# Optimization experiments

Measured on AMD Instinct MI355X. Metric: run time of the kernel, lower is better.

Reference implementation:

```python
import jax, jax.numpy as jnp
import numpy as np

B, N, D, H, C = 32, 128, 5000, 256, 4  # trees, nodes/tree, input_size_rumor, hidden, rumor_classes


def setup_inputs() -> dict:
    key = jax.random.key(0)
    ks = jax.random.split(key, 24)
    scale = 0.05  # xavier-like scale (module calls init_weight with xavier_uniform_)
    inp = {"x": jax.random.normal(ks[0], (B, N, D), dtype=jnp.float32)}
    names = ["Er", "Wsr_r", "Usr_r", "Wsr_z", "Usr_z", "Wsr_h", "Usr_h",
             "Wr_r", "Ur_r", "Usr2r_r", "Wr_z", "Ur_z", "Usr2r_z",
             "Wr_h", "Ur_h", "Usr2r_h"]
    shapes = [(H, D)] + [(H, H)] * 15
    for i, (n, s) in enumerate(zip(names, shapes)):
        inp[n] = jax.random.normal(ks[i + 1], s, dtype=jnp.float32) * scale
    inp["Vr"] = jax.random.normal(ks[17], (C, H), dtype=jnp.float32) * scale
    inp["br"] = jnp.zeros((C, 1), dtype=jnp.float32)
    # Tree structure: nodes in topological order; slot 0 = zero initial state,
    # node j is stored at slot j+1, parents[:, i] is the SLOT of node i's parent.
    rng = np.random.default_rng(0)
    pslot = np.zeros((B, N), dtype=np.int64)  # root's parent slot = 0 (zeros)
    for i in range(1, N):
        pslot[:, i] = rng.integers(1, i + 1, size=B)  # parent is an earlier node
    has_child = np.zeros((B, N), dtype=bool)
    for i in range(1, N):
        has_child[np.arange(B), pslot[:, i] - 1] = True
    inp["parents"] = jnp.asarray(pslot)
    inp["is_leaf"] = jnp.asarray(~has_child)
    return inp


def _tree_gru(x_tilde, parents, Wsr_r, Usr_r, Wsr_z, Usr_z, Wsr_h, Usr_h,
              Wr_r, Ur_r, Usr2r_r, Wr_z, Ur_z, Usr2r_z, Wr_h, Ur_h, Usr2r_h):
    """x_tilde: [B,N,H] embedded node features; parents: [B,N] parent SLOT ids.
    Returns h_rumor for every node: [B,N,H]. Same math as MultiModel.rumor_forward,
    with the Python recursion replaced by a scan over topologically-ordered nodes,
    vectorized across the batch of trees."""
    Bq, Nq, Hq = x_tilde.shape
    S0 = jnp.zeros((Bq, Nq + 1, Hq), x_tilde.dtype)  # slot 0 = initial zero state

    def step(carry, xs):
        S_sh, S_ru = carry  # [B, N+1, H] stored shared/rumor states
        xt, p, i = xs       # xt: [B,H], p: [B] parent slot, i: node index
        idx = p[:, None, None]
        hsp = jnp.take_along_axis(S_sh, idx, axis=1)[:, 0]  # [B,H] parent shared state
        hrp = jnp.take_along_axis(S_ru, idx, axis=1)[:, 0]  # [B,H] parent rumor state
        # shared GRU cell
        r_sh = jax.nn.sigmoid(xt @ Wsr_r.T + hsp @ Usr_r.T)
        z_sh = jax.nn.sigmoid(xt @ Wsr_z.T + hsp @ Usr_z.T)
        h_sh_t = jnp.tanh(xt @ Wsr_h.T + (hsp * r_sh) @ Usr_h.T)
        h_sh = (1 - z_sh) * hsp + z_sh * h_sh_t
        # rumor GRU cell (conditioned on shared state)
        r_ru = jax.nn.sigmoid(xt @ Wr_r.T + hrp @ Ur_r.T + h_sh @ Usr2r_r.T)
        z_ru = jax.nn.sigmoid(xt @ Wr_z.T + hrp @ Ur_z.T + h_sh @ Usr2r_z.T)
        h_ru_t = jnp.tanh(xt @ Wr_h.T + (hrp * r_ru) @ Ur_h.T + h_sh @ Usr2r_h.T)
        h_ru = (1 - z_ru) * hrp + z_ru * h_ru_t
        S_sh = S_sh.at[:, i + 1, :].set(h_sh)
        S_ru = S_ru.at[:, i + 1, :].set(h_ru)
        return (S_sh, S_ru), None

    xs = (jnp.swapaxes(x_tilde, 0, 1), parents.T, jnp.arange(Nq))
    (S_sh, S_ru), _ = jax.lax.scan(step, (S0, S0), xs)
    return S_ru[:, 1:, :]


def reference(x, Er, Wsr_r, Usr_r, Wsr_z, Usr_z, Wsr_h, Usr_h,
              Wr_r, Ur_r, Usr2r_r, Wr_z, Ur_z, Usr2r_z, Wr_h, Ur_h, Usr2r_h,
              Vr, br, parents, is_leaf):
    x_tilde = jnp.einsum('bnd,hd->bnh', x, Er)  # Er @ x for every node
    H_ru = _tree_gru(x_tilde, parents, Wsr_r, Usr_r, Wsr_z, Usr_z, Wsr_h, Usr_h,
                     Wr_r, Ur_r, Usr2r_r, Wr_z, Ur_z, Usr2r_z, Wr_h, Ur_h, Usr2r_h)
    # max over leaf node hidden vectors (torch.max over cat of leaf vectors)
    neg = jnp.finfo(H_ru.dtype).min
    hmax = jnp.where(is_leaf[:, :, None], H_ru, neg).max(axis=1)  # [B,H]
    logits = hmax @ Vr.T + br[:, 0]  # [B,C]
    return jax.nn.softmax(logits, axis=-1)
```

## Files before the change

### kernel.cpp

```cpp
#include <hip/hip_runtime.h>
#include <hip/hip_bf16.h>
#include <math.h>


#define H_DIM 256
#define N_NODES 128
#define B_TREES 32
#define MAXL 128
#define TPB 2
#define GRID_WGS 512

typedef short bf16x8 __attribute__((ext_vector_type(8)));
typedef float f32x4 __attribute__((ext_vector_type(4)));

__device__ __forceinline__ float sigmoidf_(float x) {
    return 1.0f / (1.0f + expf(-x));
}
__device__ __forceinline__ unsigned bfp(float x) {
    unsigned u = __float_as_uint(x);
    return (u + 0x7fffu + ((u >> 16) & 1u)) >> 16;
}
__device__ __forceinline__ float bflo(unsigned w) { return __uint_as_float(w << 16); }
__device__ __forceinline__ float bfhi(unsigned w) { return __uint_as_float(w & 0xffff0000u); }

__device__ __forceinline__ void unpack8(uint4 v, float* f) {
    f[0] = bflo(v.x); f[1] = bfhi(v.x);
    f[2] = bflo(v.y); f[3] = bfhi(v.y);
    f[4] = bflo(v.z); f[5] = bfhi(v.z);
    f[6] = bflo(v.w); f[7] = bfhi(v.w);
}

__device__ __forceinline__ float coh_load(const float* p) {
    return __hip_atomic_load(p, __ATOMIC_RELAXED, __HIP_MEMORY_SCOPE_AGENT);
}
__device__ __forceinline__ void coh_store(float* p, float v) {
    __hip_atomic_store(p, v, __ATOMIC_RELAXED, __HIP_MEMORY_SCOPE_AGENT);
}
__device__ __forceinline__ unsigned coh_loadu(const unsigned* p) {
    return __hip_atomic_load(p, __ATOMIC_RELAXED, __HIP_MEMORY_SCOPE_AGENT);
}
__device__ __forceinline__ void coh_storeu(unsigned* p, unsigned v) {
    __hip_atomic_store(p, v, __ATOMIC_RELAXED, __HIP_MEMORY_SCOPE_AGENT);
}

__global__ __launch_bounds__(256) void gemm_mfma_nt(
    const float* __restrict__ A, const float* __restrict__ B,
    float* __restrict__ C, int K, int ldc, int Kc, int zStride) {
    __shared__ short As[64][40];
    __shared__ short Bs[64][40];
    const int tid = threadIdx.x;
    const int bm = blockIdx.x, bn = blockIdx.y;
    const int z = blockIdx.z;
    const int k_begin = z * Kc;
    const int k_end = (k_begin + Kc < K) ? (k_begin + Kc) : K;
    float* Cz = C + (size_t)z * zStride;
    const int row = tid >> 2;
    const int quad = tid & 3;
    const int wave = tid >> 6;
    const int lane = tid & 63;
    const int lm = lane & 15;
    const int kq = lane >> 4;

    f32x4 acc[4];
#pragma unroll
    for (int i = 0; i < 4; ++i) acc[i] = (f32x4){0.f, 0.f, 0.f, 0.f};

    for (int k0 = k_begin; k0 < k_end; k0 += 32) {
        const int kbase = k0 + quad * 8;
        {
            float a8[8];
            const float* Ap = A + (size_t)(bm * 64 + row) * K + kbase;
            if (kbase + 8 <= k_end) {
                const float4 v0 = *(const float4*)Ap;
                const float4 v1 = *(const float4*)(Ap + 4);
                a8[0] = v0.x; a8[1] = v0.y; a8[2] = v0.z; a8[3] = v0.w;
                a8[4] = v1.x; a8[5] = v1.y; a8[6] = v1.z; a8[7] = v1.w;
            } else {
#pragma unroll
                for (int i = 0; i < 8; ++i)
                    a8[i] = (kbase + i < k_end) ? Ap[i] : 0.f;
            }
            uint4 v;
            v.x = bfp(a8[0]) | (bfp(a8[1]) << 16);
            v.y = bfp(a8[2]) | (bfp(a8[3]) << 16);
            v.z = bfp(a8[4]) | (bfp(a8[5]) << 16);
            v.w = bfp(a8[6]) | (bfp(a8[7]) << 16);
            *(uint4*)&As[row][quad * 8] = v;
        }
        {
            float b8[8];
            const float* Bp = B + (size_t)(bn * 64 + row) * K + kbase;
            if (kbase + 8 <= k_end) {
                const float4 v0 = *(const float4*)Bp;
                const float4 v1 = *(const float4*)(Bp + 4);
                b8[0] = v0.x; b8[1] = v0.y; b8[2] = v0.z; b8[3] = v0.w;
                b8[4] = v1.x; b8[5] = v1.y; b8[6] = v1.z; b8[7] = v1.w;
            } else {
#pragma unroll
                for (int i = 0; i < 8; ++i)
                    b8[i] = (kbase + i < k_end) ? Bp[i] : 0.f;
            }
            uint4 v;
            v.x = bfp(b8[0]) | (bfp(b8[1]) << 16);
            v.y = bfp(b8[2]) | (bfp(b8[3]) << 16);
            v.z = bfp(b8[4]) | (bfp(b8[5]) << 16);
            v.w = bfp(b8[6]) | (bfp(b8[7]) << 16);
            *(uint4*)&Bs[row][quad * 8] = v;
        }
        __syncthreads();
        const bf16x8 af = *(const bf16x8*)&As[wave * 16 + lm][kq * 8];
#pragma unroll
        for (int nt = 0; nt < 4; ++nt) {
            const bf16x8 bf = *(const bf16x8*)&Bs[nt * 16 + lm][kq * 8];
            acc[nt] = __builtin_amdgcn_mfma_f32_16x16x32_bf16(af, bf, acc[nt], 0, 0, 0);
        }
        __syncthreads();
    }
#pragma unroll
    for (int nt = 0; nt < 4; ++nt) {
#pragma unroll
        for (int r = 0; r < 4; ++r) {
            const int gm = bm * 64 + wave * 16 + kq * 4 + r;
            const int gn = bn * 64 + nt * 16 + lm;
            Cz[(size_t)gm * ldc + gn] = acc[nt][r];
        }
    }
}

__global__ __launch_bounds__(256) void gemm_mfma_w6(
    const float* __restrict__ A,
    const float* __restrict__ B0, const float* __restrict__ B1,
    const float* __restrict__ B2, const float* __restrict__ B3,
    const float* __restrict__ B4, const float* __restrict__ B5,
    float* __restrict__ C, int ldc) {
    __shared__ short As[64][40];
    __shared__ short Bs[64][40];
    const int tid = threadIdx.x;
    const int bm = blockIdx.x, bn = blockIdx.y;
    const float* Bsel[6] = {B0, B1, B2, B3, B4, B5};
    const int row = tid >> 2;
    const int quad = tid & 3;
    const int wave = tid >> 6;
    const int lane = tid & 63;
    const int lm = lane & 15;
    const int kq = lane >> 4;
    const float* Brow = Bsel[bn >> 2] + (size_t)((bn & 3) * 64 + row) * 256;
    const float* Arow = A + (size_t)(bm * 64 + row) * 256;

    f32x4 acc[4];
#pragma unroll
    for (int i = 0; i < 4; ++i) acc[i] = (f32x4){0.f, 0.f, 0.f, 0.f};

#pragma unroll
    for (int kt = 0; kt < 8; ++kt) {
        const int kbase = kt * 32 + quad * 8;
        {
            const float4 v0 = *(const float4*)(Arow + kbase);
            const float4 v1 = *(const float4*)(Arow + kbase + 4);
            uint4 v;
            v.x = bfp(v0.x) | (bfp(v0.y) << 16);
            v.y = bfp(v0.z) | (bfp(v0.w) << 16);
            v.z = bfp(v1.x) | (bfp(v1.y) << 16);
            v.w = bfp(v1.z) | (bfp(v1.w) << 16);
            *(uint4*)&As[row][quad * 8] = v;
        }
        {
            const float4 v0 = *(const float4*)(Brow + kbase);
            const float4 v1 = *(const float4*)(Brow + kbase + 4);
            uint4 v;
            v.x = bfp(v0.x) | (bfp(v0.y) << 16);
            v.y = bfp(v0.z) | (bfp(v0.w) << 16);
            v.z = bfp(v1.x) | (bfp(v1.y) << 16);
            v.w = bfp(v1.z) | (bfp(v1.w) << 16);
            *(uint4*)&Bs[row][quad * 8] = v;
        }
        __syncthreads();
        const bf16x8 af = *(const bf16x8*)&As[wave * 16 + lm][kq * 8];
#pragma unroll
        for (int nt = 0; nt < 4; ++nt) {
            const bf16x8 bf = *(const bf16x8*)&Bs[nt * 16 + lm][kq * 8];
            acc[nt] = __builtin_amdgcn_mfma_f32_16x16x32_bf16(af, bf, acc[nt], 0, 0, 0);
        }
        __syncthreads();
    }
#pragma unroll
    for (int nt = 0; nt < 4; ++nt) {
#pragma unroll
        for (int r = 0; r < 4; ++r) {
            const int gm = bm * 64 + wave * 16 + kq * 4 + r;
            const int gn = bn * 64 + nt * 16 + lm;
            C[(size_t)gm * ldc + gn] = acc[nt][r];
        }
    }
}

__global__ __launch_bounds__(256) void reduce4_k(
    const float* __restrict__ Pp, float* __restrict__ xt) {
    const int i = (blockIdx.x * 256 + threadIdx.x) * 4;
    const float4 a = *(const float4*)(Pp + i);
    const float4 b = *(const float4*)(Pp + 1048576 + i);
    const float4 c = *(const float4*)(Pp + 2097152 + i);
    const float4 d = *(const float4*)(Pp + 3145728 + i);
    float4 s;
    s.x = a.x + b.x + c.x + d.x;
    s.y = a.y + b.y + c.y + d.y;
    s.z = a.z + b.z + c.z + d.z;
    s.w = a.w + b.w + c.w + d.w;
    *(float4*)(xt + i) = s;
}

__global__ __launch_bounds__(256) void transpose_pack_u(
    const float* __restrict__ U0, const float* __restrict__ U1,
    const float* __restrict__ U2, const float* __restrict__ U3,
    const float* __restrict__ U4, const float* __restrict__ U5,
    const float* __restrict__ U6, const float* __restrict__ U7,
    const float* __restrict__ U8, uint4* __restrict__ UTb) {
    const float* Us[9] = {U0, U1, U2, U3, U4, U5, U6, U7, U8};
    const int jb = blockIdx.x;
    const int m = blockIdx.y;
    const int h = threadIdx.x;
    const float* U = Us[m] + (size_t)h * 256 + jb * 8;
    uint4 v;
    v.x = bfp(U[0]) | (bfp(U[1]) << 16);
    v.y = bfp(U[2]) | (bfp(U[3]) << 16);
    v.z = bfp(U[4]) | (bfp(U[5]) << 16);
    v.w = bfp(U[6]) | (bfp(U[7]) << 16);
    UTb[(size_t)(m * 32 + jb) * 256 + h] = v;
}

__global__ __launch_bounds__(256) void build_schedule(
    const int* __restrict__ parents, int* __restrict__ sched,
    int* __restrict__ level_off, int* __restrict__ gstart,
    int* __restrict__ gend, int* __restrict__ ngrp,
    unsigned* __restrict__ ready) {
    __shared__ unsigned char depth[B_TREES][N_NODES];
    __shared__ int counts[MAXL];
    __shared__ int base[MAXL + 1];
    const int tid = threadIdx.x;
    for (int k = tid; k < B_TREES * N_NODES; k += 256)
        coh_storeu(&ready[k], 0u);
    for (int k = tid; k < MAXL; k += 256) counts[k] = 0;
    __syncthreads();
    if (tid < B_TREES) {
        depth[tid][0] = 0;
        for (int i = 1; i < N_NODES; ++i) {
            const int p = parents[tid * N_NODES + i];
            depth[tid][i] = (unsigned char)(depth[tid][p - 1] + 1);
        }
    }
    __syncthreads();
    for (int k = tid; k < B_TREES * N_NODES; k += 256)
        atomicAdd(&counts[depth[k >> 7][k & 127]], 1);
    __syncthreads();
    if (tid == 0) {
        int acc = 0;
        int nl = 0;
        for (int l = 0; l < MAXL; ++l) {
            base[l] = acc;
            acc += counts[l];
            if (counts[l] > 0) nl = l + 1;
        }
        base[MAXL] = acc;
        level_off[MAXL + 1] = nl;
        int ng = 0;
        for (int l = 0; l < nl; ++l) {
            for (int s = base[l]; s < base[l + 1]; s += TPB) {
                gstart[ng] = s;
                gend[ng] = (s + TPB < base[l + 1]) ? s + TPB : base[l + 1];
                ++ng;
            }
        }
        *ngrp = ng;
    }
    __syncthreads();
    for (int k = tid; k <= MAXL; k += 256) level_off[k] = base[k];
    for (int k = tid; k < MAXL; k += 256) counts[k] = 0;
    __syncthreads();
    for (int k = tid; k < B_TREES * N_NODES; k += 256) {
        const int d = depth[k >> 7][k & 127];
        const int pos = base[d] + atomicAdd(&counts[d], 1);
        sched[pos] = k;
    }
}

__global__ __launch_bounds__(256, 2) void tree_scan_df(
    const float* __restrict__ P, const uint4* __restrict__ UTb,
    const int* __restrict__ parents,
    const int* __restrict__ sched,
    const int* __restrict__ gstart, const int* __restrict__ gend,
    const int* __restrict__ ngrp, unsigned* __restrict__ ready,
    float* __restrict__ Ssh, float* __restrict__ Sru) {
    const int h = threadIdx.x;
    const int wg = blockIdx.x;
    __shared__ float hsp_s[H_DIM][TPB];
    __shared__ float hrp_s[H_DIM][TPB];
    __shared__ float aux_s[H_DIM][TPB];
    __shared__ float hsh_s[H_DIM][TPB];

    const uint4* __restrict__ U0b = UTb + 0 * 8192;
    const uint4* __restrict__ U1b = UTb + 1 * 8192;
    const uint4* __restrict__ U2b = UTb + 2 * 8192;
    const uint4* __restrict__ U3b = UTb + 3 * 8192;
    const uint4* __restrict__ U4b = UTb + 4 * 8192;
    const uint4* __restrict__ U5b = UTb + 5 * 8192;
    const uint4* __restrict__ U6b = UTb + 6 * 8192;
    const uint4* __restrict__ U7b = UTb + 7 * 8192;
    const uint4* __restrict__ U8b = UTb + 8 * 8192;

    const int ng = ngrp[0];
    for (int g = wg; g < ng; g += GRID_WGS) {
        const int s = gstart[g];
        const int e = gend[g];
        if (h < e - s) {
            const int nd = sched[s + h];
            const int p = parents[nd];
            if (p != 0) {
                const unsigned* f = &ready[(nd & ~127) + p - 1];
                while (coh_loadu(f) == 0u) __builtin_amdgcn_s_sleep(1);
            }
        }
        __syncthreads();

        int  node[TPB];
        bool val[TPB];
        float phs[TPB], phr[TPB];
#pragma unroll
        for (int t = 0; t < TPB; ++t) {
            const int idx = s + t;
            val[t] = idx < e;
            const int nd = val[t] ? sched[idx] : sched[s];
            node[t] = nd;
            const int p = parents[nd];
            float hs = 0.f, hr = 0.f;
            if (p != 0) {
                const size_t pr = ((size_t)((nd & ~127) + p - 1)) * H_DIM + h;
                hs = coh_load(&Ssh[pr]);
                hr = coh_load(&Sru[pr]);
            }
            phs[t] = hs;
            phr[t] = hr;
        }
        *(float2*)&hsp_s[h][0] = make_float2(phs[0], phs[1]);
        *(float2*)&hrp_s[h][0] = make_float2(phr[0], phr[1]);
        __syncthreads();

        float pr_[TPB], pz_[TPB];
#pragma unroll
        for (int t = 0; t < TPB; ++t) {
            const float* Pi = P + (size_t)node[t] * 1536;
            pr_[t] = Pi[h];
            pz_[t] = Pi[256 + h];
        }
        float dr[TPB] = {0.f, 0.f};
        float dz[TPB] = {0.f, 0.f};
#pragma unroll 4
        for (int jb = 0; jb < 32; ++jb) {
            const uint4 w0 = U0b[jb * 256 + h];
            const uint4 w1 = U1b[jb * 256 + h];
            float a[8], c[8];
            unpack8(w0, a);
            unpack8(w1, c);
#pragma unroll
            for (int q = 0; q < 8; ++q) {
                const float2 hv = *(const float2*)&hsp_s[jb * 8 + q][0];
                dr[0] = fmaf(a[q], hv.x, dr[0]);
                dr[1] = fmaf(a[q], hv.y, dr[1]);
                dz[0] = fmaf(c[q], hv.x, dz[0]);
                dz[1] = fmaf(c[q], hv.y, dz[1]);
            }
        }
        float z_sh[TPB], vsh[TPB];
#pragma unroll
        for (int t = 0; t < TPB; ++t) {
            const float r_sh = sigmoidf_(pr_[t] + dr[t]);
            z_sh[t] = sigmoidf_(pz_[t] + dz[t]);
            vsh[t] = phs[t] * r_sh;
        }
        *(float2*)&aux_s[h][0] = make_float2(vsh[0], vsh[1]);
        __syncthreads();

        float ph_[TPB];
#pragma unroll
        for (int t = 0; t < TPB; ++t)
            ph_[t] = P[(size_t)node[t] * 1536 + 512 + h];
        float dh[TPB] = {0.f, 0.f};
#pragma unroll 8
        for (int jb = 0; jb < 32; ++jb) {
            const uint4 w2 = U2b[jb * 256 + h];
            float a[8];
            unpack8(w2, a);
#pragma unroll
            for (int q = 0; q < 8; ++q) {
                const float2 hv = *(const float2*)&aux_s[jb * 8 + q][0];
                dh[0] = fmaf(a[q], hv.x, dh[0]);
                dh[1] = fmaf(a[q], hv.y, dh[1]);
            }
        }
        float hsh[TPB];
#pragma unroll
        for (int t = 0; t < TPB; ++t) {
            const float hsh_t = tanhf(ph_[t] + dh[t]);
            hsh[t] = (1.f - z_sh[t]) * phs[t] + z_sh[t] * hsh_t;
            if (val[t])
                coh_store(&Ssh[(size_t)node[t] * H_DIM + h], hsh[t]);
        }
        *(float2*)&hsh_s[h][0] = make_float2(hsh[0], hsh[1]);
        __syncthreads();

        float pru_[TPB], pzu_[TPB];
#pragma unroll
        for (int t = 0; t < TPB; ++t) {
            const float* Pi = P + (size_t)node[t] * 1536;
            pru_[t] = Pi[768 + h];
            pzu_[t] = Pi[1024 + h];
        }
        float er[TPB] = {0.f, 0.f};
        float ez[TPB] = {0.f, 0.f};
        float fr[TPB] = {0.f, 0.f};
        float fz[TPB] = {0.f, 0.f};
#pragma unroll 2
        for (int jb = 0; jb < 32; ++jb) {
            const uint4 w3 = U3b[jb * 256 + h];
            const uint4 w4 = U4b[jb * 256 + h];
            const uint4 w6 = U6b[jb * 256 + h];
            const uint4 w7 = U7b[jb * 256 + h];
            float a3[8], a4[8], a6[8], a7[8];
            unpack8(w3, a3);
            unpack8(w4, a4);
            unpack8(w6, a6);
            unpack8(w7, a7);
#pragma unroll
            for (int q = 0; q < 8; ++q) {
                const float2 hr2 = *(const float2*)&hrp_s[jb * 8 + q][0];
                const float2 hs2 = *(const float2*)&hsh_s[jb * 8 + q][0];
                er[0] = fmaf(a3[q], hr2.x, er[0]);
                er[1] = fmaf(a3[q], hr2.y, er[1]);
                ez[0] = fmaf(a4[q], hr2.x, ez[0]);
                ez[1] = fmaf(a4[q], hr2.y, ez[1]);
                fr[0] = fmaf(a6[q], hs2.x, fr[0]);
                fr[1] = fmaf(a6[q], hs2.y, fr[1]);
                fz[0] = fmaf(a7[q], hs2.x, fz[0]);
                fz[1] = fmaf(a7[q], hs2.y, fz[1]);
            }
        }
        float z_ru[TPB], v2[TPB];
#pragma unroll
        for (int t = 0; t < TPB; ++t) {
            const float r_ru = sigmoidf_(pru_[t] + er[t] + fr[t]);
            z_ru[t] = sigmoidf_(pzu_[t] + ez[t] + fz[t]);
            v2[t] = phr[t] * r_ru;
        }
        *(float2*)&aux_s[h][0] = make_float2(v2[0], v2[1]);
        __syncthreads();

        float phu_[TPB];
#pragma unroll
        for (int t = 0; t < TPB; ++t)
            phu_[t] = P[(size_t)node[t] * 1536 + 1280 + h];
        float eh[TPB] = {0.f, 0.f};
        float fh[TPB] = {0.f, 0.f};
#pragma unroll 4
        for (int jb = 0; jb < 32; ++jb) {
            const uint4 w5 = U5b[jb * 256 + h];
            const uint4 w8 = U8b[jb * 256 + h];
            float a5[8], a8[8];
            unpack8(w5, a5);
            unpack8(w8, a8);
#pragma unroll
            for (int q = 0; q < 8; ++q) {
                const float2 v4 = *(const float2*)&aux_s[jb * 8 + q][0];
                const float2 s4 = *(const float2*)&hsh_s[jb * 8 + q][0];
                eh[0] = fmaf(a5[q], v4.x, eh[0]);
                eh[1] = fmaf(a5[q], v4.y, eh[1]);
                fh[0] = fmaf(a8[q], s4.x, fh[0]);
                fh[1] = fmaf(a8[q], s4.y, fh[1]);
            }
        }
#pragma unroll
        for (int t = 0; t < TPB; ++t) {
            const float hru_t = tanhf(phu_[t] + eh[t] + fh[t]);
            const float h_ru = (1.f - z_ru[t]) * phr[t] + z_ru[t] * hru_t;
            if (val[t])
                coh_store(&Sru[(size_t)node[t] * H_DIM + h], h_ru);
        }
        __syncthreads();
        if (h < e - s)
            coh_storeu(&ready[sched[s + h]], 1u);
        __syncthreads();
    }
}

__global__ __launch_bounds__(256) void epilogue_k(
    const float* __restrict__ Sru, const int* __restrict__ is_leaf,
    const float* __restrict__ Vr, const float* __restrict__ br,
    float* __restrict__ out) {
    const int b = blockIdx.x;
    const int h = threadIdx.x;
    float m = -3.402823466e38f;
    for (int n = 0; n < N_NODES; ++n) {
        const float v = Sru[((size_t)b * N_NODES + n) * H_DIM + h];
        if (is_leaf[b * N_NODES + n] != 0) m = fmaxf(m, v);
    }
    __shared__ float hm[H_DIM];
    __shared__ float lg[4];
    hm[h] = m;
    __syncthreads();
    if (h < 4) {
        float acc = br[h];
#pragma unroll 8
        for (int j = 0; j < H_DIM; ++j) acc = fmaf(Vr[h * 256 + j], hm[j], acc);
        lg[h] = acc;
    }
    __syncthreads();
    if (h == 0) {
        const float mx = fmaxf(fmaxf(lg[0], lg[1]), fmaxf(lg[2], lg[3]));
        const float e0 = expf(lg[0] - mx);
        const float e1 = expf(lg[1] - mx);
        const float e2 = expf(lg[2] - mx);
        const float e3 = expf(lg[3] - mx);
        const float s = e0 + e1 + e2 + e3;
        out[b * 4 + 0] = e0 / s;
        out[b * 4 + 1] = e1 / s;
        out[b * 4 + 2] = e2 / s;
        out[b * 4 + 3] = e3 / s;
    }
}

extern "C" void kernel_launch(void* const* d_in, const int* in_sizes, int n_in,
                              void* d_out, int out_size, void* d_ws, size_t ws_size,
                              hipStream_t stream) {
    const float* x      = (const float*)d_in[0];
    const float* Er     = (const float*)d_in[1];
    const float* Wsr_r  = (const float*)d_in[2];
    const float* Usr_r  = (const float*)d_in[3];
    const float* Wsr_z  = (const float*)d_in[4];
    const float* Usr_z  = (const float*)d_in[5];
    const float* Wsr_h  = (const float*)d_in[6];
    const float* Usr_h  = (const float*)d_in[7];
    const float* Wr_r   = (const float*)d_in[8];
    const float* Ur_r   = (const float*)d_in[9];
    const float* Usr2r_r= (const float*)d_in[10];
    const float* Wr_z   = (const float*)d_in[11];
    const float* Ur_z   = (const float*)d_in[12];
    const float* Usr2r_z= (const float*)d_in[13];
    const float* Wr_h   = (const float*)d_in[14];
    const float* Ur_h   = (const float*)d_in[15];
    const float* Usr2r_h= (const float*)d_in[16];
    const float* Vr     = (const float*)d_in[17];
    const float* br     = (const float*)d_in[18];
    const int*   parents= (const int*)d_in[19];
    const int*   is_leaf= (const int*)d_in[20];
    float* out = (float*)d_out;

    float* ws = (float*)d_ws;
    float* xt   = ws;
    float* P    = xt + 1048576;
    float* Wcat = P + 6291456;
    uint4* UTb  = (uint4*)(Wcat + 393216);
    float* Ssh  = (float*)(UTb + 73728);
    float* Sru  = Ssh + 1048576;
    int*   sched     = (int*)(Sru + 1048576);
    int*   level_off = sched + 4096;
    unsigned* ready  = (unsigned*)(level_off + 192);
    int*   gstart    = (int*)(ready + 4096);
    int*   gend      = gstart + 4096;
    int*   ngrp      = gend + 4096;

    dim3 blk(256);

    gemm_mfma_nt<<<dim3(64, 4, 4), blk, 0, stream>>>(x, Er, P, 5000, 256,
                                                     1280, 1048576);
    reduce4_k<<<dim3(1024), blk, 0, stream>>>(P, xt);

    gemm_mfma_w6<<<dim3(64, 24), blk, 0, stream>>>(
        xt, Wsr_r, Wsr_z, Wsr_h, Wr_r, Wr_z, Wr_h, P, 1536);

    transpose_pack_u<<<dim3(32, 9), blk, 0, stream>>>(
        Usr_r, Usr_z, Usr_h, Ur_r, Ur_z, Ur_h, Usr2r_r, Usr2r_z, Usr2r_h, UTb);

    build_schedule<<<dim3(1), blk, 0, stream>>>(parents, sched, level_off,
                                                gstart, gend, ngrp, ready);

    void* args[] = {(void*)&P, (void*)&UTb, (void*)&parents, (void*)&sched,
                    (void*)&gstart, (void*)&gend, (void*)&ngrp, (void*)&ready,
                    (void*)&Ssh, (void*)&Sru};
    (void)hipLaunchCooperativeKernel((const void*)tree_scan_df,
                                     dim3(GRID_WGS), blk, args, 0, stream);

    epilogue_k<<<dim3(B_TREES), blk, 0, stream>>>(Sru, is_leaf, Vr, br, out);
}
```

Before: 842.2 us.

## Replace level-ordered node groups with heavy-path chain scheduling in tree scan

Decomposes each tree into longest-path chains (each node continues to its tallest child) and assigns one chain per workgroup. The chain's state stays in shared memory between consecutive nodes, so a node no longer has to wait on a global ready flag or reload its parent from global memory. The workgroup count drops from 512 to 256 and each workgroup now handles one node at a time instead of two. The risk is lower parallelism and a less balanced load, because chains have very different lengths and the critical path is now set by the longest chain.

New measurement: 998.8 us. 1.19x slower.

```diff
diff --git a/kernel.cpp b/kernel.cpp
--- a/kernel.cpp
+++ b/kernel.cpp
@@ -7,8 +7,7 @@
 #define N_NODES 128
 #define B_TREES 32
 #define MAXL 128
-#define TPB 2
-#define GRID_WGS 512
+#define GRID_WGS 256
 
 typedef short bf16x8 __attribute__((ext_vector_type(8)));
 typedef float f32x4 __attribute__((ext_vector_type(4)));
@@ -228,14 +227,15 @@
     UTb[(size_t)(m * 32 + jb) * 256 + h] = v;
 }
 
-__global__ __launch_bounds__(256) void build_schedule(
-    const int* __restrict__ parents, int* __restrict__ sched,
-    int* __restrict__ level_off, int* __restrict__ gstart,
-    int* __restrict__ gend, int* __restrict__ ngrp,
+__global__ __launch_bounds__(256) void build_chains(
+    const int* __restrict__ parents, int* __restrict__ nextn,
+    int* __restrict__ chstart, int* __restrict__ nchain,
     unsigned* __restrict__ ready) {
     __shared__ unsigned char depth[B_TREES][N_NODES];
+    __shared__ unsigned char height[B_TREES][N_NODES];
+    __shared__ short cont[B_TREES][N_NODES];
     __shared__ int counts[MAXL];
-    __shared__ int base[MAXL + 1];
+    __shared__ int base[MAXL];
     const int tid = threadIdx.x;
     for (int k = tid; k < B_TREES * N_NODES; k += 256)
         coh_storeu(&ready[k], 0u);
@@ -243,59 +243,61 @@
     __syncthreads();
     if (tid < B_TREES) {
         depth[tid][0] = 0;
+        for (int i = 1; i < N_NODES; ++i)
+            depth[tid][i] = (unsigned char)(depth[tid][parents[tid * N_NODES + i] - 1] + 1);
+        for (int i = 0; i < N_NODES; ++i) { height[tid][i] = 0; cont[tid][i] = -1; }
+        for (int i = N_NODES - 1; i >= 1; --i) {
+            const int p = parents[tid * N_NODES + i] - 1;
+            if ((int)height[tid][i] + 1 > (int)height[tid][p])
+                height[tid][p] = (unsigned char)(height[tid][i] + 1);
+        }
         for (int i = 1; i < N_NODES; ++i) {
-            const int p = parents[tid * N_NODES + i];
-            depth[tid][i] = (unsigned char)(depth[tid][p - 1] + 1);
-        }
-    }
-    __syncthreads();
-    for (int k = tid; k < B_TREES * N_NODES; k += 256)
-        atomicAdd(&counts[depth[k >> 7][k & 127]], 1);
+            const int p = parents[tid * N_NODES + i] - 1;
+            if (cont[tid][p] < 0 || height[tid][i] > height[tid][cont[tid][p]])
+                cont[tid][p] = (short)i;
+        }
+        for (int i = 0; i < N_NODES; ++i)
+            nextn[tid * N_NODES + i] =
+                (cont[tid][i] >= 0) ? tid * N_NODES + (int)cont[tid][i] : -1;
+    }
+    __syncthreads();
+    for (int k = tid; k < B_TREES * N_NODES; k += 256) {
+        const int t = k >> 7, i = k & 127;
+        const bool isStart = (i == 0) || (cont[t][parents[k] - 1] != (short)i);
+        if (isStart) atomicAdd(&counts[depth[t][i]], 1);
+    }
     __syncthreads();
     if (tid == 0) {
         int acc = 0;
-        int nl = 0;
-        for (int l = 0; l < MAXL; ++l) {
-            base[l] = acc;
-            acc += counts[l];
-            if (counts[l] > 0) nl = l + 1;
-        }
-        base[MAXL] = acc;
-        level_off[MAXL + 1] = nl;
-        int ng = 0;
-        for (int l = 0; l < nl; ++l) {
-            for (int s = base[l]; s < base[l + 1]; s += TPB) {
-                gstart[ng] = s;
-                gend[ng] = (s + TPB < base[l + 1]) ? s + TPB : base[l + 1];
-                ++ng;
-            }
-        }
-        *ngrp = ng;
-    }
-    __syncthreads();
-    for (int k = tid; k <= MAXL; k += 256) level_off[k] = base[k];
+        for (int l = 0; l < MAXL; ++l) { base[l] = acc; acc += counts[l]; }
+        *nchain = acc;
+    }
+    __syncthreads();
     for (int k = tid; k < MAXL; k += 256) counts[k] = 0;
     __syncthreads();
     for (int k = tid; k < B_TREES * N_NODES; k += 256) {
-        const int d = depth[k >> 7][k & 127];
-        const int pos = base[d] + atomicAdd(&counts[d], 1);
-        sched[pos] = k;
-    }
-}
-
-__global__ __launch_bounds__(256, 2) void tree_scan_df(
+        const int t = k >> 7, i = k & 127;
+        const bool isStart = (i == 0) || (cont[t][parents[k] - 1] != (short)i);
+        if (isStart) {
+            const int d = depth[t][i];
+            const int pos = base[d] + atomicAdd(&counts[d], 1);
+            chstart[pos] = k;
+        }
+    }
+}
+
+__global__ __launch_bounds__(256, 1) void tree_scan_chain(
     const float* __restrict__ P, const uint4* __restrict__ UTb,
     const int* __restrict__ parents,
-    const int* __restrict__ sched,
-    const int* __restrict__ gstart, const int* __restrict__ gend,
-    const int* __restrict__ ngrp, unsigned* __restrict__ ready,
+    const int* __restrict__ chstart, const int* __restrict__ nextn,
+    const int* __restrict__ nchain, unsigned* __restrict__ ready,
     float* __restrict__ Ssh, float* __restrict__ Sru) {
     const int h = threadIdx.x;
     const int wg = blockIdx.x;
-    __shared__ float hsp_s[H_DIM][TPB];
-    __shared__ float hrp_s[H_DIM][TPB];
-    __shared__ float aux_s[H_DIM][TPB];
-    __shared__ float hsh_s[H_DIM][TPB];
+    __shared__ float hsp_s[H_DIM];
+    __shared__ float hrp_s[H_DIM];
+    __shared__ float aux_s[H_DIM];
+    __shared__ float hsh_s[H_DIM];
 
     const uint4* __restrict__ U0b = UTb + 0 * 8192;
     const uint4* __restrict__ U1b = UTb + 1 * 8192;
@@ -307,186 +309,121 @@
     const uint4* __restrict__ U7b = UTb + 7 * 8192;
     const uint4* __restrict__ U8b = UTb + 8 * 8192;
 
-    const int ng = ngrp[0];
-    for (int g = wg; g < ng; g += GRID_WGS) {
-        const int s = gstart[g];
-        const int e = gend[g];
-        if (h < e - s) {
-            const int nd = sched[s + h];
-            const int p = parents[nd];
-            if (p != 0) {
-                const unsigned* f = &ready[(nd & ~127) + p - 1];
-                while (coh_loadu(f) == 0u) __builtin_amdgcn_s_sleep(1);
+    const int nc = nchain[0];
+    for (int c = wg; c < nc; c += GRID_WGS) {
+        int nd = chstart[c];
+        const int p0 = parents[nd];
+        if (h == 0 && p0 != 0) {
+            const unsigned* f = &ready[(nd & ~127) + p0 - 1];
+            while (coh_loadu(f) == 0u) __builtin_amdgcn_s_sleep(1);
+        }
+        __syncthreads();
+        float phs = 0.f, phr = 0.f;
+        if (p0 != 0) {
+            const size_t pr = ((size_t)((nd & ~127) + p0 - 1)) * H_DIM + h;
+            phs = coh_load(&Ssh[pr]);
+            phr = coh_load(&Sru[pr]);
+        }
+        hsp_s[h] = phs;
+        hrp_s[h] = phr;
+        __syncthreads();
+
+        while (nd >= 0) {
+            const float* Pi = P + (size_t)nd * 1536;
+            const float pr_ = Pi[h];
+            const float pz_ = Pi[256 + h];
+            float dr = 0.f, dz = 0.f;
+#pragma unroll 4
+            for (int jb = 0; jb < 32; ++jb) {
+                const uint4 w0 = U0b[jb * 256 + h];
+                const uint4 w1 = U1b[jb * 256 + h];
+                float a[8], c8[8];
+                unpack8(w0, a);
+                unpack8(w1, c8);
+#pragma unroll
+                for (int q = 0; q < 8; ++q) {
+                    const float hv = hsp_s[jb * 8 + q];
+                    dr = fmaf(a[q], hv, dr);
+                    dz = fmaf(c8[q], hv, dz);
+                }
             }
-        }
-        __syncthreads();
-
-        int  node[TPB];
-        bool val[TPB];
-        float phs[TPB], phr[TPB];
-#pragma unroll
-        for (int t = 0; t < TPB; ++t) {
-            const int idx = s + t;
-            val[t] = idx < e;
-            const int nd = val[t] ? sched[idx] : sched[s];
-            node[t] = nd;
-            const int p = parents[nd];
-            float hs = 0.f, hr = 0.f;
-            if (p != 0) {
-                const size_t pr = ((size_t)((nd & ~127) + p - 1)) * H_DIM + h;
-                hs = coh_load(&Ssh[pr]);
-                hr = coh_load(&Sru[pr]);
+            const float r_sh = sigmoidf_(pr_ + dr);
+            const float z_sh = sigmoidf_(pz_ + dz);
+            aux_s[h] = phs * r_sh;
+            __syncthreads();
+
+            const float ph_ = Pi[512 + h];
+            float dh = 0.f;
+#pragma unroll 8
+            for (int jb = 0; jb < 32; ++jb) {
+                const uint4 w2 = U2b[jb * 256 + h];
+                float a[8];
+                unpack8(w2, a);
+#pragma unroll
+                for (int q = 0; q < 8; ++q)
+                    dh = fmaf(a[q], aux_s[jb * 8 + q], dh);
             }
-            phs[t] = hs;
-            phr[t] = hr;
-        }
-        *(float2*)&hsp_s[h][0] = make_float2(phs[0], phs[1]);
-        *(float2*)&hrp_s[h][0] = make_float2(phr[0], phr[1]);
-        __syncthreads();
-
-        float pr_[TPB], pz_[TPB];
-#pragma unroll
-        for (int t = 0; t < TPB; ++t) {
-            const float* Pi = P + (size_t)node[t] * 1536;
-            pr_[t] = Pi[h];
-            pz_[t] = Pi[256 + h];
-        }
-        float dr[TPB] = {0.f, 0.f};
-        float dz[TPB] = {0.f, 0.f};
+            const float hsh_t = tanhf(ph_ + dh);
+            const float hsh = (1.f - z_sh) * phs + z_sh * hsh_t;
+            coh_store(&Ssh[(size_t)nd * H_DIM + h], hsh);
+            hsh_s[h] = hsh;
+            hsp_s[h] = hsh;
+            __syncthreads();
+
+            const float pru_ = Pi[768 + h];
+            const float pzu_ = Pi[1024 + h];
+            float er = 0.f, ez = 0.f, fr = 0.f, fz = 0.f;
+#pragma unroll 2
+            for (int jb = 0; jb < 32; ++jb) {
+                const uint4 w3 = U3b[jb * 256 + h];
+                const uint4 w4 = U4b[jb * 256 + h];
+                const uint4 w6 = U6b[jb * 256 + h];
+                const uint4 w7 = U7b[jb * 256 + h];
+                float a3[8], a4[8], a6[8], a7[8];
+                unpack8(w3, a3);
+                unpack8(w4, a4);
+                unpack8(w6, a6);
+                unpack8(w7, a7);
+#pragma unroll
+                for (int q = 0; q < 8; ++q) {
+                    const float hrv = hrp_s[jb * 8 + q];
+                    const float hsv = hsh_s[jb * 8 + q];
+                    er = fmaf(a3[q], hrv, er);
+                    ez = fmaf(a4[q], hrv, ez);
+                    fr = fmaf(a6[q], hsv, fr);
+                    fz = fmaf(a7[q], hsv, fz);
+                }
+            }
+            const float r_ru = sigmoidf_(pru_ + er + fr);
+            const float z_ru = sigmoidf_(pzu_ + ez + fz);
+            aux_s[h] = phr * r_ru;
+            __syncthreads();
+
+            const float phu_ = Pi[1280 + h];
+            float eh = 0.f, fh = 0.f;
 #pragma unroll 4
-        for (int jb = 0; jb < 32; ++jb) {
-            const uint4 w0 = U0b[jb * 256 + h];
-            const uint4 w1 = U1b[jb * 256 + h];
-            float a[8], c[8];
-            unpack8(w0, a);
-            unpack8(w1, c);
-#pragma unroll
-            for (int q = 0; q < 8; ++q) {
-                const float2 hv = *(const float2*)&hsp_s[jb * 8 + q][0];
-                dr[0] = fmaf(a[q], hv.x, dr[0]);
-                dr[1] = fmaf(a[q], hv.y, dr[1]);
-                dz[0] = fmaf(c[q], hv.x, dz[0]);
-                dz[1] = fmaf(c[q], hv.y, dz[1]);
+            for (int jb = 0; jb < 32; ++jb) {
+                const uint4 w5 = U5b[jb * 256 + h];
+                const uint4 w8 = U8b[jb * 256 + h];
+                float a5[8], a8v[8];
+                unpack8(w5, a5);
+                unpack8(w8, a8v);
+#pragma unroll
+                for (int q = 0; q < 8; ++q) {
+                    eh = fmaf(a5[q], aux_s[jb * 8 + q], eh);
+                    fh = fmaf(a8v[q], hsh_s[jb * 8 + q], fh);
+                }
             }
-        }
-        float z_sh[TPB], vsh[TPB];
-#pragma unroll
-        for (int t = 0; t < TPB; ++t) {
-            const float r_sh = sigmoidf_(pr_[t] + dr[t]);
-            z_sh[t] = sigmoidf_(pz_[t] + dz[t]);
-            vsh[t] = phs[t] * r_sh;
-        }
-        *(float2*)&aux_s[h][0] = make_float2(vsh[0], vsh[1]);
-        __syncthreads();
-
-        float ph_[TPB];
-#pragma unroll
-        for (int t = 0; t < TPB; ++t)
-            ph_[t] = P[(size_t)node[t] * 1536 + 512 + h];
-        float dh[TPB] = {0.f, 0.f};
-#pragma unroll 8
-        for (int jb = 0; jb < 32; ++jb) {
-            const uint4 w2 = U2b[jb * 256 + h];
-            float a[8];
-            unpack8(w2, a);
-#pragma unroll
-            for (int q = 0; q < 8; ++q) {
-                const float2 hv = *(const float2*)&aux_s[jb * 8 + q][0];
-                dh[0] = fmaf(a[q], hv.x, dh[0]);
-                dh[1] = fmaf(a[q], hv.y, dh[1]);
-            }
-        }
-        float hsh[TPB];
-#pragma unroll
-        for (int t = 0; t < TPB; ++t) {
-            const float hsh_t = tanhf(ph_[t] + dh[t]);
-            hsh[t] = (1.f - z_sh[t]) * phs[t] + z_sh[t] * hsh_t;
-            if (val[t])
-                coh_store(&Ssh[(size_t)node[t] * H_DIM + h], hsh[t]);
-        }
-        *(float2*)&hsh_s[h][0] = make_float2(hsh[0], hsh[1]);
-        __syncthreads();
-
-        float pru_[TPB], pzu_[TPB];
-#pragma unroll
-        for (int t = 0; t < TPB; ++t) {
-            const float* Pi = P + (size_t)node[t] * 1536;
-            pru_[t] = Pi[768 + h];
-            pzu_[t] = Pi[1024 + h];
-        }
-        float er[TPB] = {0.f, 0.f};
-        float ez[TPB] = {0.f, 0.f};
-        float fr[TPB] = {0.f, 0.f};
-        float fz[TPB] = {0.f, 0.f};
-#pragma unroll 2
-        for (int jb = 0; jb < 32; ++jb) {
-            const uint4 w3 = U3b[jb * 256 + h];
-            const uint4 w4 = U4b[jb * 256 + h];
-            const uint4 w6 = U6b[jb * 256 + h];
-            const uint4 w7 = U7b[jb * 256 + h];
-            float a3[8], a4[8], a6[8], a7[8];
-            unpack8(w3, a3);
-            unpack8(w4, a4);
-            unpack8(w6, a6);
-            unpack8(w7, a7);
-#pragma unroll
-            for (int q = 0; q < 8; ++q) {
-                const float2 hr2 = *(const float2*)&hrp_s[jb * 8 + q][0];
-                const float2 hs2 = *(const float2*)&hsh_s[jb * 8 + q][0];
-                er[0] = fmaf(a3[q], hr2.x, er[0]);
-                er[1] = fmaf(a3[q], hr2.y, er[1]);
-                ez[0] = fmaf(a4[q], hr2.x, ez[0]);
-                ez[1] = fmaf(a4[q], hr2.y, ez[1]);
-                fr[0] = fmaf(a6[q], hs2.x, fr[0]);
-                fr[1] = fmaf(a6[q], hs2.y, fr[1]);
-                fz[0] = fmaf(a7[q], hs2.x, fz[0]);
-                fz[1] = fmaf(a7[q], hs2.y, fz[1]);
-            }
-        }
-        float z_ru[TPB], v2[TPB];
-#pragma unroll
-        for (int t = 0; t < TPB; ++t) {
-            const float r_ru = sigmoidf_(pru_[t] + er[t] + fr[t]);
-            z_ru[t] = sigmoidf_(pzu_[t] + ez[t] + fz[t]);
-            v2[t] = phr[t] * r_ru;
-        }
-        *(float2*)&aux_s[h][0] = make_float2(v2[0], v2[1]);
-        __syncthreads();
-
-        float phu_[TPB];
-#pragma unroll
-        for (int t = 0; t < TPB; ++t)
-            phu_[t] = P[(size_t)node[t] * 1536 + 1280 + h];
-        float eh[TPB] = {0.f, 0.f};
-        float fh[TPB] = {0.f, 0.f};
-#pragma unroll 4
-        for (int jb = 0; jb < 32; ++jb) {
-            const uint4 w5 = U5b[jb * 256 + h];
-            const uint4 w8 = U8b[jb * 256 + h];
-            float a5[8], a8[8];
-            unpack8(w5, a5);
-            unpack8(w8, a8);
-#pragma unroll
-            for (int q = 0; q < 8; ++q) {
-                const float2 v4 = *(const float2*)&aux_s[jb * 8 + q][0];
-                const float2 s4 = *(const float2*)&hsh_s[jb * 8 + q][0];
-                eh[0] = fmaf(a5[q], v4.x, eh[0]);
-                eh[1] = fmaf(a5[q], v4.y, eh[1]);
-                fh[0] = fmaf(a8[q], s4.x, fh[0]);
-                fh[1] = fmaf(a8[q], s4.y, fh[1]);
-            }
-        }
-#pragma unroll
-        for (int t = 0; t < TPB; ++t) {
-            const float hru_t = tanhf(phu_[t] + eh[t] + fh[t]);
-            const float h_ru = (1.f - z_ru[t]) * phr[t] + z_ru[t] * hru_t;
-            if (val[t])
-                coh_store(&Sru[(size_t)node[t] * H_DIM + h], h_ru);
-        }
-        __syncthreads();
-        if (h < e - s)
-            coh_storeu(&ready[sched[s + h]], 1u);
-        __syncthreads();
+            const float hru_t = tanhf(phu_ + eh + fh);
+            const float h_ru = (1.f - z_ru) * phr + z_ru * hru_t;
+            coh_store(&Sru[(size_t)nd * H_DIM + h], h_ru);
+            hrp_s[h] = h_ru;
+            __syncthreads();
+            if (h == 0) coh_storeu(&ready[nd], 1u);
+            phs = hsh;
+            phr = h_ru;
+            nd = nextn[nd];
+        }
     }
 }
 
@@ -559,12 +496,10 @@
     uint4* UTb  = (uint4*)(Wcat + 393216);
     float* Ssh  = (float*)(UTb + 73728);
     float* Sru  = Ssh + 1048576;
-    int*   sched     = (int*)(Sru + 1048576);
-    int*   level_off = sched + 4096;
-    unsigned* ready  = (unsigned*)(level_off + 192);
-    int*   gstart    = (int*)(ready + 4096);
-    int*   gend      = gstart + 4096;
-    int*   ngrp      = gend + 4096;
+    int*   nextn     = (int*)(Sru + 1048576);
+    int*   chstart   = nextn + 4096;
+    int*   nchain    = chstart + 4096;
+    unsigned* ready  = (unsigned*)(nchain + 16);
 
     dim3 blk(256);
 
@@ -578,13 +513,13 @@
     transpose_pack_u<<<dim3(32, 9), blk, 0, stream>>>(
         Usr_r, Usr_z, Usr_h, Ur_r, Ur_z, Ur_h, Usr2r_r, Usr2r_z, Usr2r_h, UTb);
 
-    build_schedule<<<dim3(1), blk, 0, stream>>>(parents, sched, level_off,
-                                                gstart, gend, ngrp, ready);
-
-    void* args[] = {(void*)&P, (void*)&UTb, (void*)&parents, (void*)&sched,
-                    (void*)&gstart, (void*)&gend, (void*)&ngrp, (void*)&ready,
+    build_chains<<<dim3(1), blk, 0, stream>>>(parents, nextn, chstart,
+                                              nchain, ready);
+
+    void* args[] = {(void*)&P, (void*)&UTb, (void*)&parents, (void*)&chstart,
+                    (void*)&nextn, (void*)&nchain, (void*)&ready,
                     (void*)&Ssh, (void*)&Sru};
-    (void)hipLaunchCooperativeKernel((const void*)tree_scan_df,
+    (void)hipLaunchCooperativeKernel((const void*)tree_scan_chain,
                                      dim3(GRID_WGS), blk, args, 0, stream);
 
     epilogue_k<<<dim3(B_TREES), blk, 0, stream>>>(Sru, is_leaf, Vr, br, out);
```
